# Optimization experiments

Measured on AMD Instinct MI355X. Metric: run time of the kernel, lower is better.

## Reference

```python
import jax, jax.numpy as jnp
import numpy as np

ALPHA = 0.2
TOP_K = 32

def setup_inputs() -> dict:
    key = jax.random.key(0)
    k1, k2, k3, k4, k5 = jax.random.split(key, 5)
    B, T, N, D = 2, 12, 8192, 256
    X = jax.random.normal(k1, (B, T, N, D), dtype=jnp.float32)
    E1 = jax.random.normal(k2, (N, D), dtype=jnp.float32)
    E2 = jax.random.normal(k3, (N, D), dtype=jnp.float32)
    theta1 = jax.random.normal(k4, (D, D), dtype=jnp.float32)
    theta2 = jax.random.normal(k5, (D, D), dtype=jnp.float32)
    a = jnp.float32(1.0)
    return {"X": X, "E1": E1, "E2": E2, "theta1": theta1, "theta2": theta2, "a": a}

def reference(X, E1, E2, theta1, theta2, a):
    # X: [B, T, N, D]
    N = X.shape[2]
    X0 = X.mean(axis=1)[0]  # [N, D], mean over time, first batch element
    # Row-wise L2 normalize (F.normalize with eps=1e-12)
    norm = jnp.maximum(jnp.linalg.norm(X0, axis=1, keepdims=True), 1e-12)
    X_norm = X0 / norm
    sim = X_norm @ X_norm.T  # [N, N] cosine similarity
    sim = sim * (1.0 - jnp.eye(N, dtype=sim.dtype))  # zero diagonal
    topk_vals, topk_idx = jax.lax.top_k(sim, TOP_K)  # [N, K]
    rows = jnp.arange(N)[:, None]
    A_base = jnp.zeros_like(sim).at[rows, topk_idx].set(topk_vals)
    # Adaptive dependency matrix
    M1 = jnp.tanh(ALPHA * (E1 @ theta1))  # [N, D]
    M2 = jnp.tanh(ALPHA * (E2 @ theta2))  # [N, D]
    diff = M1 @ M2.T - M2 @ M1.T  # [N, N], antisymmetric
    adaptive = jax.nn.relu(jnp.tanh(a * diff))
    return adaptive * A_base
```

## Files before the change

kernel.cpp:

```cpp
#include <hip/hip_runtime.h>
#include <hip/hip_bf16.h>
#include <hip/hip_fp16.h>
#include <float.h>
#include <math.h>

#define NN 8192
#define DD 256
#define TT 12
#define TOPK 32
#define NQ 4
#define CAP 56
#define UCAP 64
#define TAU0 0.146875f
#define B2 2.2e-3f
#define DIFFCUT 3.0f

typedef __attribute__((ext_vector_type(8))) _Float16 f16x8;
typedef __attribute__((ext_vector_type(16))) float f32x16;
typedef __attribute__((ext_vector_type(4))) float f32x4;

__device__ __forceinline__ unsigned short f2h(float x) {
    __half h = __float2half(x);
    return *(unsigned short*)&h;
}
__device__ __forceinline__ float h2f(unsigned short v) {
    __half h = *(__half*)&v;
    return __half2float(h);
}

__global__ __launch_bounds__(256) void k_mean_norm(const float* __restrict__ X,
                                                   float* __restrict__ Xn,
                                                   unsigned short* __restrict__ Xpk) {
    const int row = blockIdx.x;
    const int d = threadIdx.x;
    const float* base = X + (size_t)row * DD + d;
    double s = 0.0;
#pragma unroll
    for (int t = 0; t < TT; ++t) s += (double)base[(size_t)t * NN * DD];
    const double mean = s / 12.0;

    double ss = mean * mean;
#pragma unroll
    for (int o = 32; o > 0; o >>= 1) ss += __shfl_down(ss, o, 64);
    __shared__ double wss[4];
    const int lane = threadIdx.x & 63, w = threadIdx.x >> 6;
    if (lane == 0) wss[w] = ss;
    __syncthreads();
    double nrm = sqrt(wss[0] + wss[1] + wss[2] + wss[3]);
    if (nrm < 1e-12) nrm = 1e-12;
    const float xv = (float)(mean / nrm);
    Xn[(size_t)row * DD + d] = xv;

    const int cb = row >> 5;
    const int ks = d >> 4;
    const int l = (row & 31) + 32 * ((d >> 3) & 1);
    const int e = d & 7;
    Xpk[(((size_t)cb * 16 + ks) * 64 + l) * 8 + e] = f2h(xv);
}

__global__ __launch_bounds__(256, 3) void k_simcand_M(
    const unsigned short* __restrict__ Xpk,
    const float* __restrict__ E1, const float* __restrict__ E2,
    const float* __restrict__ th1, const float* __restrict__ th2,
    float* __restrict__ M1, float* __restrict__ M2,
    unsigned int* __restrict__ Mpk,
    unsigned short* __restrict__ cand, float* __restrict__ candv,
    int* __restrict__ counts, float* __restrict__ out) {
    __shared__ __align__(16) unsigned char smem[16384];

    const int tid = threadIdx.x;

    if (blockIdx.x < 1024) {
        int* cnt = (int*)smem;
        unsigned short* lst = (unsigned short*)(smem + 128);
        float* lstv = (float*)(smem + 128 + 32 * CAP * 2);

        const int nt = tid >> 6, lane = tid & 63;
        const int simIdx = blockIdx.x;
        const int bx = simIdx & 255;
        const int quarter = simIdx >> 8;
        const int r0 = bx * 32;

        for (int i = tid; i < 32; i += 256) cnt[i] = 0;

        const f32x4 zz = {0.f, 0.f, 0.f, 0.f};
        f32x4* zp = (f32x4*)out + ((size_t)simIdx * 16384) + tid;

        f16x8 afr[16];
        {
            const size_t abase = ((size_t)bx * 16) * 512 + lane * 8;
#pragma unroll
            for (int ks = 0; ks < 16; ++ks)
                afr[ks] = *(const f16x8*)(Xpk + abase + ks * 512);
        }
        __syncthreads();

        const int rowL = (lane >> 5) << 2;
        const int colL = lane & 31;

        f16x8 bA[8], bB[8];
        {
            const size_t bb0 = ((size_t)(quarter * 64 + nt) * 16) * 512 + lane * 8;
#pragma unroll
            for (int ks = 0; ks < 8; ++ks)
                bA[ks] = *(const f16x8*)(Xpk + bb0 + ks * 512);
        }

#pragma unroll
        for (int c = 0; c < 16; ++c) {
            const int cbB = quarter * 64 + c * 4 + nt;
            const int gcol = cbB * 32 + colL;
            const size_t bbase = ((size_t)cbB * 16) * 512 + lane * 8;

#pragma unroll
            for (int ks = 0; ks < 8; ++ks)
                bB[ks] = *(const f16x8*)(Xpk + bbase + (8 + ks) * 512);

            f32x16 acc;
#pragma unroll
            for (int q = 0; q < 16; ++q) acc[q] = 0.f;

#pragma unroll
            for (int ks = 0; ks < 8; ++ks)
                acc = __builtin_amdgcn_mfma_f32_32x32x16_f16(afr[ks], bA[ks], acc, 0, 0, 0);

            if (c < 15) {
                const size_t bn = ((size_t)(cbB + 4) * 16) * 512 + lane * 8;
#pragma unroll
                for (int ks = 0; ks < 8; ++ks)
                    bA[ks] = *(const f16x8*)(Xpk + bn + ks * 512);
            }

#pragma unroll
            for (int ks = 0; ks < 8; ++ks)
                acc = __builtin_amdgcn_mfma_f32_32x32x16_f16(afr[8 + ks], bB[ks], acc, 0, 0, 0);

#pragma unroll
            for (int q = 0; q < 4; ++q)
                __builtin_nontemporal_store(zz, zp + (c * 4 + q) * 256);

#pragma unroll
            for (int reg = 0; reg < 16; ++reg) {
                const float v = acc[reg];
                if (v > TAU0) {
                    const int rl = rowL + (reg & 3) + ((reg >> 2) << 3);
                    if (r0 + rl != gcol) {
                        const int idx = atomicAdd(&cnt[rl], 1);
                        if (idx < CAP) {
                            lst[rl * CAP + idx] = (unsigned short)gcol;
                            lstv[rl * CAP + idx] = v;
                        }
                    }
                }
            }
        }
        __syncthreads();
        for (int i = tid; i < 32; i += 256) {
            int n = cnt[i];
            counts[(r0 + i) * NQ + quarter] = n > CAP ? CAP : n;
        }
        for (int i = tid; i < 32 * CAP; i += 256) {
            const int rl = i / CAP, k = i % CAP;
            int n = cnt[rl];
            if (n > CAP) n = CAP;
            if (k < n) {
                const size_t o = ((size_t)(r0 + rl) * NQ + quarter) * CAP + k;
                cand[o] = lst[rl * CAP + k];
                candv[o] = lstv[rl * CAP + k];
            }
        }
    } else {
        float* e1 = (float*)smem;
        float* e2 = (float*)(smem + 8192);
        const int r0 = (blockIdx.x - 1024) * 8;
        {
            const f32x4* E14 = (const f32x4*)(E1 + (size_t)r0 * DD);
            const f32x4* E24 = (const f32x4*)(E2 + (size_t)r0 * DD);
            f32x4* e14 = (f32x4*)e1;
            f32x4* e24 = (f32x4*)e2;
            for (int i = tid; i < 512; i += 256) {
                e14[i] = E14[i];
                e24[i] = E24[i];
            }
        }
        __syncthreads();
        const int j = tid;
        float a1[8], a2[8];
#pragma unroll
        for (int r = 0; r < 8; ++r) { a1[r] = 0.f; a2[r] = 0.f; }
        for (int k = 0; k < DD; k += 4) {
            float t1[4], t2[4];
#pragma unroll
            for (int kk = 0; kk < 4; ++kk) {
                t1[kk] = th1[(size_t)(k + kk) * DD + j];
                t2[kk] = th2[(size_t)(k + kk) * DD + j];
            }
#pragma unroll
            for (int r = 0; r < 8; ++r) {
                const f32x4 ev1 = *(const f32x4*)&e1[r * DD + k];
                const f32x4 ev2 = *(const f32x4*)&e2[r * DD + k];
                a1[r] += ev1.x * t1[0];
                a1[r] += ev1.y * t1[1];
                a1[r] += ev1.z * t1[2];
                a1[r] += ev1.w * t1[3];
                a2[r] += ev2.x * t2[0];
                a2[r] += ev2.y * t2[1];
                a2[r] += ev2.z * t2[2];
                a2[r] += ev2.w * t2[3];
            }
        }
#pragma unroll
        for (int r = 0; r < 8; ++r) {
            const float m1v = tanhf(0.2f * a1[r]);
            const float m2v = tanhf(0.2f * a2[r]);
            M1[(size_t)(r0 + r) * DD + j] = m1v;
            M2[(size_t)(r0 + r) * DD + j] = m2v;
            Mpk[(size_t)(r0 + r) * DD + j] =
                ((unsigned)f2h(m2v) << 16) | (unsigned)f2h(m1v);
        }
    }
}

__global__ __launch_bounds__(256) void k_refine(
    const float* __restrict__ Xn, const unsigned short* __restrict__ cand,
    const float* __restrict__ candv, const int* __restrict__ counts,
    const float* __restrict__ M1, const float* __restrict__ M2,
    const unsigned int* __restrict__ Mpk, const float* __restrict__ a_ptr,
    float* __restrict__ out) {
    __shared__ float xi[DD], m1i[DD], m2i[DD];
    __shared__ unsigned short cidx[NQ * CAP];
    __shared__ float cs[NQ * CAP];
    __shared__ int carr[NQ], offs[NQ + 1];
    __shared__ unsigned short uidx[UCAP];
    __shared__ float ue[UCAP];
    __shared__ int nUs, ms;
    __shared__ float wv[TOPK];
    __shared__ int wj[TOPK];

    const int i = blockIdx.x, t = threadIdx.x;

    xi[t]  = Xn[(size_t)i * DD + t];
    m1i[t] = M1[(size_t)i * DD + t];
    m2i[t] = M2[(size_t)i * DD + t];
    if (t < NQ) {
        int n = counts[i * NQ + t];
        carr[t] = n < 0 ? 0 : (n > CAP ? CAP : n);
    }
    if (t < TOPK) { wv[t] = 0.f; wj[t] = i; }
    if (t == 0) { nUs = 0; ms = 0; }
    __syncthreads();
    if (t == 0) {
        int s = 0;
#pragma unroll
        for (int q = 0; q < NQ; ++q) { offs[q] = s; s += carr[q]; }
        offs[NQ] = s;
    }
    __syncthreads();
    const int nc = offs[NQ];
#pragma unroll
    for (int q = 0; q < NQ; ++q)
        if (t < carr[q]) {
            const size_t o = ((size_t)i * NQ + q) * CAP + t;
            cidx[offs[q] + t] = cand[o];
            cs[offs[q] + t] = candv[o];
        }
    __syncthreads();

    if (t < nc) {
        const float vc = cs[t];
        int possAbove = 0, certAbove = 0;
        for (int k = 0; k < nc; ++k) {
            const float vk = cs[k];
            possAbove += (vk >= vc - B2);
            certAbove += (vk > vc + B2);
        }
        possAbove -= 1;
        if (possAbove <= TOPK - 1) {
            const int slot = atomicAdd(&ms, 1);
            wv[slot] = vc;
            wj[slot] = cidx[t];
        } else if (certAbove < TOPK) {
            const int p = atomicAdd(&nUs, 1);
            if (p < UCAP) uidx[p] = cidx[t];
        }
    }
    __syncthreads();
    const int m = ms;
    int nU = nUs;
    if (nU > UCAP) nU = UCAP;

    if (nU > 0) {
        const int dl = t & 15, cg = t >> 4;
        for (int base = 0; base < nU; base += 16) {
            const int c = base + cg;
            float p = 0.f;
            if (c < nU) {
                const int j = uidx[c];
                const f32x4* xj4 = (const f32x4*)(Xn + (size_t)j * DD) + dl * 4;
                const f32x4* xi4 = (const f32x4*)xi + dl * 4;
#pragma unroll
                for (int q = 0; q < 4; ++q) {
                    const f32x4 A = xi4[q], B = xj4[q];
                    p += A.x * B.x;
                    p += A.y * B.y;
                    p += A.z * B.z;
                    p += A.w * B.w;
                }
            }
#pragma unroll
            for (int o = 1; o < 16; o <<= 1) p += __shfl_xor(p, o, 64);
            if (c < nU && dl == 0) ue[c] = p;
        }
        __syncthreads();
        if (t < nU && m < TOPK) {
            const float vc = ue[t];
            const int jc = uidx[t];
            int r = 0;
            for (int k = 0; k < nU; ++k) {
                const float vk = ue[k];
                r += (vk > vc) || (vk == vc && uidx[k] < jc);
            }
            if (r < TOPK - m) {
                wv[m + r] = vc;
                wj[m + r] = jc;
            }
        }
        __syncthreads();
    }

    const float a = *a_ptr;
    const int g = t >> 3, lg = t & 7;
    const int j = wj[g];
    const float v = wv[g];

    float p1 = 0.f;
    {
        const uint4* mp = (const uint4*)(Mpk + (size_t)j * DD) + lg * 8;
#pragma unroll
        for (int q = 0; q < 8; ++q) {
            const uint4 u = mp[q];
            const int d = lg * 32 + q * 4;
            p1 += m1i[d + 0] * h2f((unsigned short)(u.x >> 16)) -
                  m2i[d + 0] * h2f((unsigned short)(u.x & 0xffff));
            p1 += m1i[d + 1] * h2f((unsigned short)(u.y >> 16)) -
                  m2i[d + 1] * h2f((unsigned short)(u.y & 0xffff));
            p1 += m1i[d + 2] * h2f((unsigned short)(u.z >> 16)) -
                  m2i[d + 2] * h2f((unsigned short)(u.z & 0xffff));
            p1 += m1i[d + 3] * h2f((unsigned short)(u.w >> 16)) -
                  m2i[d + 3] * h2f((unsigned short)(u.w & 0xffff));
        }
    }
#pragma unroll
    for (int o = 4; o > 0; o >>= 1) p1 += __shfl_xor(p1, o, 64);

    float diff = p1;
    if (fabsf(diff) < DIFFCUT) {
        const f32x4* m1j4 = (const f32x4*)(M1 + (size_t)j * DD) + lg * 8;
        const f32x4* m2j4 = (const f32x4*)(M2 + (size_t)j * DD) + lg * 8;
        float p = 0.f;
        const int dbase = lg * 32;
#pragma unroll
        for (int q = 0; q < 8; ++q) {
            const f32x4 b1 = m1j4[q], b2 = m2j4[q];
            const int d = dbase + q * 4;
            p += m1i[d + 0] * b2.x - m2i[d + 0] * b1.x;
            p += m1i[d + 1] * b2.y - m2i[d + 1] * b1.y;
            p += m1i[d + 2] * b2.z - m2i[d + 2] * b1.z;
            p += m1i[d + 3] * b2.w - m2i[d + 3] * b1.w;
        }
#pragma unroll
        for (int o = 4; o > 0; o >>= 1) p += __shfl_xor(p, o, 64);
        diff = p;
    }
    if (lg == 0 && j != i) {
        float ad = tanhf(a * diff);
        ad = ad > 0.f ? ad : 0.f;
        out[(size_t)i * NN + j] = ad * v;
    }
}

extern "C" void kernel_launch(void* const* d_in, const int* in_sizes, int n_in,
                              void* d_out, int out_size, void* d_ws, size_t ws_size,
                              hipStream_t stream) {
    const float* X   = (const float*)d_in[0];
    const float* E1  = (const float*)d_in[1];
    const float* E2  = (const float*)d_in[2];
    const float* th1 = (const float*)d_in[3];
    const float* th2 = (const float*)d_in[4];
    const float* a   = (const float*)d_in[5];
    float* out = (float*)d_out;

    float* ws = (float*)d_ws;
    float* Xn = ws;
    float* M1 = Xn + (size_t)NN * DD;
    float* M2 = M1 + (size_t)NN * DD;
    unsigned short* Xpk = (unsigned short*)(M2 + (size_t)NN * DD);
    unsigned int* Mpk = (unsigned int*)(Xpk + (size_t)NN * DD);
    unsigned short* cand = (unsigned short*)(Mpk + (size_t)NN * DD);
    float* candv = (float*)(cand + (size_t)NN * NQ * CAP);
    int* counts = (int*)(candv + (size_t)NN * NQ * CAP);

    k_mean_norm<<<NN, 256, 0, stream>>>(X, Xn, Xpk);
    k_simcand_M<<<2048, 256, 0, stream>>>(Xpk, E1, E2, th1, th2,
                                          M1, M2, Mpk,
                                          cand, candv, counts, out);
    k_refine<<<NN, 256, 0, stream>>>(Xn, cand, candv, counts, M1, M2, Mpk, a, out);
}
```

Baseline: 230.0 us.

## Stage A tile in LDS, stop unrolling column loop, defer output zeroing

The 32-row A fragment moves from 16 f16x8 registers per lane into shared memory, and each MFMA now reads it from LDS. The column-block loop is no longer unrolled, and the zero-fill of the output block moves from inside the loop to after candidate extraction. This is meant to cut VGPR pressure so more waves fit per CU, and to keep the zero stores from competing with the compute loop. The costs are extra LDS traffic and latency on every MFMA operand, more shared memory per block, and a burst of stores at the end.

```diff
diff --git a/kernel.cpp b/kernel.cpp
--- a/kernel.cpp
+++ b/kernel.cpp
@@ -66,37 +66,33 @@
     unsigned int* __restrict__ Mpk,
     unsigned short* __restrict__ cand, float* __restrict__ candv,
     int* __restrict__ counts, float* __restrict__ out) {
-    __shared__ __align__(16) unsigned char smem[16384];
-
+    __shared__ __align__(16) unsigned char smem[27264];
     const int tid = threadIdx.x;
-
-    if (blockIdx.x < 1024) {
-        int* cnt = (int*)smem;
-        unsigned short* lst = (unsigned short*)(smem + 128);
-        float* lstv = (float*)(smem + 128 + 32 * CAP * 2);
+    const int g = blockIdx.x;
+
+    if (g < 1024) {
+        unsigned short* a_lds = (unsigned short*)smem;
+        int* cnt = (int*)(smem + 16384);
+        unsigned short* lst = (unsigned short*)(smem + 16512);
+        float* lstv = (float*)(smem + 20096);
 
         const int nt = tid >> 6, lane = tid & 63;
-        const int simIdx = blockIdx.x;
-        const int bx = simIdx & 255;
-        const int quarter = simIdx >> 8;
+        const int bx = g & 255;
+        const int quarter = g >> 8;
         const int r0 = bx * 32;
 
+        {
+            const f32x4* src = (const f32x4*)(Xpk + (size_t)bx * 8192);
+            f32x4* dst = (f32x4*)a_lds;
+#pragma unroll
+            for (int i = 0; i < 4; ++i) dst[tid + i * 256] = src[tid + i * 256];
+        }
         for (int i = tid; i < 32; i += 256) cnt[i] = 0;
-
-        const f32x4 zz = {0.f, 0.f, 0.f, 0.f};
-        f32x4* zp = (f32x4*)out + ((size_t)simIdx * 16384) + tid;
-
-        f16x8 afr[16];
-        {
-            const size_t abase = ((size_t)bx * 16) * 512 + lane * 8;
-#pragma unroll
-            for (int ks = 0; ks < 16; ++ks)
-                afr[ks] = *(const f16x8*)(Xpk + abase + ks * 512);
-        }
         __syncthreads();
 
         const int rowL = (lane >> 5) << 2;
         const int colL = lane & 31;
+        const unsigned short* arow = a_lds + lane * 8;
 
         f16x8 bA[8], bB[8];
         {
@@ -106,7 +102,7 @@
                 bA[ks] = *(const f16x8*)(Xpk + bb0 + ks * 512);
         }
 
-#pragma unroll
+#pragma unroll 1
         for (int c = 0; c < 16; ++c) {
             const int cbB = quarter * 64 + c * 4 + nt;
             const int gcol = cbB * 32 + colL;
@@ -121,8 +117,10 @@
             for (int q = 0; q < 16; ++q) acc[q] = 0.f;
 
 #pragma unroll
-            for (int ks = 0; ks < 8; ++ks)
-                acc = __builtin_amdgcn_mfma_f32_32x32x16_f16(afr[ks], bA[ks], acc, 0, 0, 0);
+            for (int ks = 0; ks < 8; ++ks) {
+                const f16x8 af = *(const f16x8*)(arow + ks * 512);
+                acc = __builtin_amdgcn_mfma_f32_32x32x16_f16(af, bA[ks], acc, 0, 0, 0);
+            }
 
             if (c < 15) {
                 const size_t bn = ((size_t)(cbB + 4) * 16) * 512 + lane * 8;
@@ -132,12 +130,10 @@
             }
 
 #pragma unroll
-            for (int ks = 0; ks < 8; ++ks)
-                acc = __builtin_amdgcn_mfma_f32_32x32x16_f16(afr[8 + ks], bB[ks], acc, 0, 0, 0);
-
-#pragma unroll
-            for (int q = 0; q < 4; ++q)
-                __builtin_nontemporal_store(zz, zp + (c * 4 + q) * 256);
+            for (int ks = 0; ks < 8; ++ks) {
+                const f16x8 af = *(const f16x8*)(arow + (8 + ks) * 512);
+                acc = __builtin_amdgcn_mfma_f32_32x32x16_f16(af, bB[ks], acc, 0, 0, 0);
+            }
 
 #pragma unroll
             for (int reg = 0; reg < 16; ++reg) {
@@ -169,10 +165,17 @@
                 candv[o] = lstv[rl * CAP + k];
             }
         }
+        {
+            const f32x4 zz = {0.f, 0.f, 0.f, 0.f};
+            f32x4* zp = (f32x4*)out + ((size_t)g * 16384) + tid;
+#pragma unroll
+            for (int q = 0; q < 64; ++q)
+                __builtin_nontemporal_store(zz, zp + q * 256);
+        }
     } else {
         float* e1 = (float*)smem;
         float* e2 = (float*)(smem + 8192);
-        const int r0 = (blockIdx.x - 1024) * 8;
+        const int r0 = (g - 1024) * 8;
         {
             const f32x4* E14 = (const f32x4*)(E1 + (size_t)r0 * DD);
             const f32x4* E24 = (const f32x4*)(E2 + (size_t)r0 * DD);
```

Measured after the change: 254.8 us. 1.11x slower.
